# Kernel optimization log

Measured on AMD Instinct MI355X. Metric: run time of the kernel, lower is better.

## Reference

```python
import jax, jax.numpy as jnp
import numpy as np

B, N, C_IN, C_OUT = 8, 4096, 64, 64
NEG_INF = -9e15
LEAKY_SLOPE = 0.01  # torch F.leaky_relu default


def setup_inputs() -> dict:
    key = jax.random.key(0)
    kx, ka, kw, kq, kk = jax.random.split(key, 5)
    X = jax.random.normal(kx, (B, N, C_IN), dtype=jnp.float32)
    A = jax.random.randint(ka, (N, N), 0, 2, dtype=jnp.int32)
    # xavier_uniform with gain=1.414 ~ scaled uniform; plain scaled normal is fine for a numeric reference
    def xavier(k, shape):
        fan_in, fan_out = shape
        bound = 1.414 * np.sqrt(6.0 / (fan_in + fan_out))
        return jax.random.uniform(k, shape, jnp.float32, -bound, bound)
    weight = xavier(kw, (C_IN, C_OUT))
    query = xavier(kq, (C_IN, C_OUT))
    key_p = xavier(kk, (C_IN, C_OUT))
    return {"X": X, "A": A, "weight": weight, "query": query, "key_p": key_p}


def reference(X, A, weight, query, key_p):
    n = X.shape[1]
    idx = jnp.arange(n)
    adj = A.at[idx, idx].set(1)  # add self-loops
    out = jnp.einsum('bni,io->bno', X, weight)
    q = jnp.einsum('bni,io->bno', X, query)
    k = jnp.einsum('bni,io->bno', X, key_p)
    att = jnp.einsum('bnd,bmd->bnm', q, k)          # QK^T, (B,N,N)
    att = jax.nn.leaky_relu(att, LEAKY_SLOPE)
    att = jnp.where(adj[None, :, :] > 0, att, NEG_INF)
    att = jax.nn.softmax(att, axis=-1)
    # dropout p=0 and/or eval mode -> identity
    return jnp.einsum('bnm,bmo->bno', att, out)
```

## Files before the change

kernel.cpp:

```cpp
#include <hip/hip_runtime.h>
#include <stdint.h>

#define BATCH 8
#define NN 4096
#define CC 64
#define MASKV -1.0e30f
#define LOG2E 1.4426950408889634f

typedef _Float16 half8 __attribute__((ext_vector_type(8)));
typedef __fp16 fp16x2 __attribute__((ext_vector_type(2)));
typedef float f32x4 __attribute__((ext_vector_type(4)));
typedef float f32x16 __attribute__((ext_vector_type(16)));

typedef __attribute__((address_space(1))) const unsigned int gu32;
typedef __attribute__((address_space(3))) unsigned int lu32;
#define GLL16(gp, lp) __builtin_amdgcn_global_load_lds( \
    (gu32*)(uintptr_t)(gp), (lu32*)(unsigned)(uintptr_t)(lp), 16, 0, 0)

__device__ __forceinline__ unsigned pk_rtz(float a, float b) {
    union { fp16x2 h; unsigned u; } r;
    r.h = __builtin_amdgcn_cvt_pkrtz(a, b);
    return r.u;
}

__global__ __launch_bounds__(256) void gat_prep(
    const float* __restrict__ X, const float* __restrict__ W0,
    const float* __restrict__ Wq, const float* __restrict__ Wk,
    const int* __restrict__ A,
    _Float16* __restrict__ qh, _Float16* __restrict__ kb,
    _Float16* __restrict__ vt, unsigned short* __restrict__ M16)
{
    __shared__ alignas(16) _Float16 WTh[3][64][72];
    __shared__ alignas(16) _Float16 WTl[3][64][72];
    const int t = threadIdx.x;
    if (blockIdx.x >= 512) {
        const int row = blockIdx.x - 512;
        const int4* ap = (const int4*)(A + (size_t)row * NN + t * 16);
        unsigned m = 0;
        #pragma unroll
        for (int j = 0; j < 4; ++j) {
            int4 a = ap[j];
            m |= (a.x != 0 ? 1u : 0u) << (4*j);
            m |= (a.y != 0 ? 1u : 0u) << (4*j + 1);
            m |= (a.z != 0 ? 1u : 0u) << (4*j + 2);
            m |= (a.w != 0 ? 1u : 0u) << (4*j + 3);
        }
        if (t == (row >> 4)) m |= 1u << (row & 15);
        M16[(size_t)row * 256 + t] = (unsigned short)m;
        return;
    }
    const float* Ws[3] = {W0, Wq, Wk};
    for (int e = t; e < 4096; e += 256) {
        int k = e >> 6, c = e & 63;
        #pragma unroll
        for (int m = 0; m < 3; ++m) {
            float w = Ws[m][e];
            _Float16 hi = (_Float16)w;
            WTh[m][c][k] = hi;
            WTl[m][c][k] = (_Float16)(w - (float)hi);
        }
    }
    __syncthreads();
    const int lane = t & 63, wv = t >> 6;
    const int cl = lane & 15, g = lane >> 4;
    int tile = blockIdx.x * 4 + wv;
    int gr = tile * 16;
    const float* xr = X + (size_t)(gr + cl) * CC;
    half8 xh[2], xl[2];
    #pragma unroll
    for (int kf = 0; kf < 2; ++kf) {
        f32x4 a0 = *(const f32x4*)(xr + g*8 + kf*32);
        f32x4 a1 = *(const f32x4*)(xr + g*8 + kf*32 + 4);
        half8 h, l;
        #pragma unroll
        for (int j = 0; j < 4; ++j) {
            _Float16 h0 = (_Float16)a0[j], h1 = (_Float16)a1[j];
            h[j]   = h0; l[j]   = (_Float16)(a0[j] - (float)h0);
            h[j+4] = h1; l[j+4] = (_Float16)(a1[j] - (float)h1);
        }
        xh[kf] = h; xl[kf] = l;
    }
    #pragma unroll
    for (int mat = 1; mat <= 2; ++mat) {
        #pragma unroll
        for (int nt = 0; nt < 4; ++nt) {
            f32x4 acc = {0.f, 0.f, 0.f, 0.f};
            #pragma unroll
            for (int kf = 0; kf < 2; ++kf) {
                half8 bh = *(const half8*)&WTh[mat][nt*16 + cl][g*8 + kf*32];
                half8 bl = *(const half8*)&WTl[mat][nt*16 + cl][g*8 + kf*32];
                acc = __builtin_amdgcn_mfma_f32_16x16x32_f16(xh[kf], bh, acc, 0, 0, 0);
                acc = __builtin_amdgcn_mfma_f32_16x16x32_f16(xl[kf], bh, acc, 0, 0, 0);
                acc = __builtin_amdgcn_mfma_f32_16x16x32_f16(xh[kf], bl, acc, 0, 0, 0);
            }
            #pragma unroll
            for (int i = 0; i < 4; ++i) {
                size_t off = (size_t)(gr + 4*g + i) * CC + nt*16 + cl;
                if (mat == 1) qh[off] = (_Float16)(acc[i] * LOG2E);
                else          kb[off] = (_Float16)acc[i];
            }
        }
    }
    {
        int b = gr >> 12, n0 = gr & (NN - 1);
        #pragma unroll
        for (int mt = 0; mt < 4; ++mt) {
            f32x4 acc = {0.f, 0.f, 0.f, 0.f};
            #pragma unroll
            for (int kf = 0; kf < 2; ++kf) {
                half8 ah = *(const half8*)&WTh[0][mt*16 + cl][g*8 + kf*32];
                half8 al = *(const half8*)&WTl[0][mt*16 + cl][g*8 + kf*32];
                acc = __builtin_amdgcn_mfma_f32_16x16x32_f16(ah, xh[kf], acc, 0, 0, 0);
                acc = __builtin_amdgcn_mfma_f32_16x16x32_f16(al, xh[kf], acc, 0, 0, 0);
                acc = __builtin_amdgcn_mfma_f32_16x16x32_f16(ah, xl[kf], acc, 0, 0, 0);
            }
            #pragma unroll
            for (int i = 0; i < 4; ++i) {
                int co = mt*16 + 4*g + i;
                vt[((size_t)b * CC + co) * NN + n0 + cl] = (_Float16)acc[i];
            }
        }
    }
}

__global__ __launch_bounds__(256) void gat_attn(
    const _Float16* __restrict__ qg,
    const _Float16* __restrict__ kf16, const _Float16* __restrict__ vtb,
    const unsigned long long* __restrict__ M,
    _Float16* __restrict__ po, float2* __restrict__ pml)
{
    __shared__ alignas(16) _Float16 Kt[2][64][64];
    __shared__ alignas(16) _Float16 Vt[2][64][64];
    __shared__ alignas(8) uint2 LUT[16];
    const int t = threadIdx.x;
    const int lane = t & 63, wv = t >> 6;
    const int q32 = lane & 31, hi = lane >> 5;
    const int blk = blockIdx.x;
    const int b  = blk & 7;
    const int sp = (blk >> 3) & 3;
    const int qb = blk >> 5;
    const int Q0 = qb * 128 + wv * 32;
    const int c0 = sp * 16;
    const int swz = (q32 & 7) << 4;

    if (t < 16) {
        unsigned n = t;
        LUT[n] = make_uint2(((n & 1u) ? 0x0000FFFFu : 0u) | ((n & 2u) ? 0xFFFF0000u : 0u),
                            ((n & 4u) ? 0x0000FFFFu : 0u) | ((n & 8u) ? 0xFFFF0000u : 0u));
    }

    const int lrow = lane >> 3;
    const int lcol = ((lane & 7) * 16) ^ (lrow << 4);
    const bool isK = (wv < 2);
    const int seg = isK ? wv : (wv - 2);
    const char* gsrc0 = isK
        ? (const char*)(kf16 + (size_t)b * NN * CC)
            + (size_t)c0 * 8192 + (size_t)seg * 4096 + lrow * 128 + lcol
        : (const char*)(vtb + (size_t)b * CC * NN)
            + (size_t)c0 * 128 + ((size_t)(seg * 32 + lrow)) * 8192 + lcol;
    const int istride = isK ? 1024 : 65536;
    const int cstride = isK ? 8192 : 128;

    auto stage = [&](int rel, int bufi) {
        const char* s = gsrc0 + (size_t)rel * cstride;
        char* d = isK ? ((char*)&Kt[bufi][0][0] + seg * 4096)
                      : ((char*)&Vt[bufi][0][0] + seg * 4096);
        #pragma unroll
        for (int i = 0; i < 4; ++i)
            GLL16(s + i * istride, d + i * 1024);
    };
    auto pkmax = [](unsigned a, unsigned b) {
        unsigned d;
        asm("v_pk_max_f16 %0, %1, %2" : "=v"(d) : "v"(a), "v"(b));
        return d;
    };

    half8 qf[4];
    {
        const _Float16* qr = qg + ((size_t)b * NN + Q0 + q32) * CC + hi * 8;
        #pragma unroll
        for (int kf = 0; kf < 4; ++kf) qf[kf] = *(const half8*)(qr + kf * 16);
    }
    const unsigned long long* Mrow = M + (size_t)(Q0 + q32) * 64 + c0;

    f32x16 o0 = {}, o1 = {};
    float m_run = 0.f, l_run = 0.f;

    stage(0, 0);
    unsigned long long cm = Mrow[0];
    __syncthreads();

    for (int kc = 0; kc < 16; ++kc) {
        const int cur = kc & 1;
        unsigned long long pmn = 0;
        if (kc < 15) {
            stage(kc + 1, cur ^ 1);
            pmn = Mrow[kc + 1];
        }

        const char* kbase = (const char*)&Kt[cur][0][0] + q32 * 128;
        __builtin_amdgcn_s_setprio(1);
        f32x16 s0 = {}, s1 = {};
        #pragma unroll
        for (int kf = 0; kf < 4; ++kf) {
            const int col = (kf * 32 + hi * 16) ^ swz;
            half8 ka0 = *(const half8*)(kbase + col);
            half8 ka1 = *(const half8*)(kbase + 4096 + col);
            s0 = __builtin_amdgcn_mfma_f32_32x32x16_f16(ka0, qf[kf], s0, 0, 0, 0);
            s1 = __builtin_amdgcn_mfma_f32_32x32x16_f16(ka1, qf[kf], s1, 0, 0, 0);
        }
        __builtin_amdgcn_s_setprio(0);

        const unsigned wlo = (unsigned)cm, whi = (unsigned)(cm >> 32);
        unsigned hm[16];
        #pragma unroll
        for (int kt = 0; kt < 2; ++kt) {
            unsigned w = kt ? whi : wlo;
            #pragma unroll
            for (int a = 0; a < 4; ++a) {
                unsigned nib = (w >> (8 * a + 4 * hi)) & 15u;
                uint2 e = LUT[nib];
                hm[kt*8 + 2*a]     = e.x;
                hm[kt*8 + 2*a + 1] = e.y;
            }
        }
        {
            unsigned sm[16];
            #pragma unroll
            for (int j = 0; j < 8; ++j) {
                sm[j]   = pk_rtz(s0[2*j], s0[2*j+1]) & hm[j];
                sm[8+j] = pk_rtz(s1[2*j], s1[2*j+1]) & hm[8+j];
            }
            unsigned u0 = pkmax(pkmax(pkmax(sm[0],sm[1]),  pkmax(sm[2],sm[3])),
                                pkmax(pkmax(sm[4],sm[5]),  pkmax(sm[6],sm[7])));
            unsigned u1 = pkmax(pkmax(pkmax(sm[8],sm[9]),  pkmax(sm[10],sm[11])),
                                pkmax(pkmax(sm[12],sm[13]),pkmax(sm[14],sm[15])));
            union { unsigned u; fp16x2 h; } tu; tu.u = pkmax(u0, u1);
            float mx = fmaxf(fmaxf((float)tu.h[0], (float)tu.h[1]), 0.f);
            mx = fmaxf(mx, __shfl_xor(mx, 32));
            if (__any(mx > m_run + 8.0f)) {
                float nm = fmaxf(m_run, mx);
                float alpha = __builtin_amdgcn_exp2f(m_run - nm);
                m_run = nm;
                l_run *= alpha;
                #pragma unroll
                for (int i = 0; i < 16; ++i) { o0[i] *= alpha; o1[i] *= alpha; }
            }
        }
        unsigned wp[16];
        #pragma unroll
        for (int j = 0; j < 8; ++j) {
            float p0 = __builtin_amdgcn_exp2f(fmaxf(s0[2*j]   - m_run, fmaf(0.01f, s0[2*j],   -m_run)));
            float p1 = __builtin_amdgcn_exp2f(fmaxf(s0[2*j+1] - m_run, fmaf(0.01f, s0[2*j+1], -m_run)));
            float p2 = __builtin_amdgcn_exp2f(fmaxf(s1[2*j]   - m_run, fmaf(0.01f, s1[2*j],   -m_run)));
            float p3 = __builtin_amdgcn_exp2f(fmaxf(s1[2*j+1] - m_run, fmaf(0.01f, s1[2*j+1], -m_run)));
            wp[j]   = pk_rtz(p0, p1) & hm[j];
            wp[8+j] = pk_rtz(p2, p3) & hm[8+j];
        }
        {
            union { unsigned u; fp16x2 h; } z; z.u = 0u;
            fp16x2 acc = z.h;
            #pragma unroll
            for (int j4 = 0; j4 < 4; ++j4) {
                union { unsigned u; fp16x2 h; } x0, x1, x2, x3;
                x0.u = wp[4*j4]; x1.u = wp[4*j4+1]; x2.u = wp[4*j4+2]; x3.u = wp[4*j4+3];
                acc += (x0.h + x1.h) + (x2.h + x3.h);
            }
            l_run += (float)acc[0] + (float)acc[1];
        }
        #pragma unroll
        for (int g4 = 0; g4 < 4; ++g4) {
            unsigned w0 = wp[4*g4+0], w1 = wp[4*g4+1];
            unsigned w2 = wp[4*g4+2], w3 = wp[4*g4+3];
            unsigned u = hi ? w0 : w2;
            unsigned v = hi ? w1 : w3;
            unsigned su = (unsigned)__shfl_xor((int)u, 32);
            unsigned sv = (unsigned)__shfl_xor((int)v, 32);
            wp[4*g4+0] = hi ? su : w0;
            wp[4*g4+1] = hi ? sv : w1;
            wp[4*g4+2] = hi ? w2 : su;
            wp[4*g4+3] = hi ? w3 : sv;
        }
        const char* vb = (const char*)&Vt[cur][0][0] + q32 * 128;
        __builtin_amdgcn_s_setprio(1);
        #pragma unroll
        for (int kc4 = 0; kc4 < 4; ++kc4) {
            union { unsigned u[4]; half8 h; } pb;
            pb.u[0] = wp[4*kc4+0]; pb.u[1] = wp[4*kc4+1];
            pb.u[2] = wp[4*kc4+2]; pb.u[3] = wp[4*kc4+3];
            const int col = (kc4 * 32 + hi * 16) ^ swz;
            half8 vf0 = *(const half8*)(vb + col);
            half8 vf1 = *(const half8*)(vb + 4096 + col);
            o0 = __builtin_amdgcn_mfma_f32_32x32x16_f16(vf0, pb.h, o0, 0, 0, 0);
            o1 = __builtin_amdgcn_mfma_f32_32x32x16_f16(vf1, pb.h, o1, 0, 0, 0);
        }
        __builtin_amdgcn_s_setprio(0);
        cm = pmn;
        if (kc < 15) __syncthreads();
    }

    float lt = l_run + __shfl_xor(l_run, 32);
    float invl = (lt > 0.f) ? 1.0f / lt : 0.f;
    size_t base = (size_t)sp * (BATCH * NN) + (size_t)b * NN + Q0 + q32;
    _Float16* orow = po + base * 64;
    #pragma unroll
    for (int a = 0; a < 4; ++a) {
        {
            uint2 ow = { pk_rtz(o0[4*a] * invl, o0[4*a+1] * invl),
                         pk_rtz(o0[4*a+2] * invl, o0[4*a+3] * invl) };
            *(uint2*)(orow + 8*a + 4*hi) = ow;
        }
        {
            uint2 ow = { pk_rtz(o1[4*a] * invl, o1[4*a+1] * invl),
                         pk_rtz(o1[4*a+2] * invl, o1[4*a+3] * invl) };
            *(uint2*)(orow + 32 + 8*a + 4*hi) = ow;
        }
    }
    if (hi == 0) pml[base] = make_float2(m_run, lt);
}

__global__ __launch_bounds__(256) void gat_comb(
    const _Float16* __restrict__ po, const float2* __restrict__ pml,
    float* __restrict__ out)
{
    int gid = blockIdx.x * 256 + threadIdx.x;
    int row = gid >> 2;
    int col = (gid & 3) * 16;
    float2 ml[4];
    float Mx = MASKV;
    #pragma unroll
    for (int s = 0; s < 4; ++s) {
        ml[s] = pml[s * (BATCH * NN) + row];
        Mx = fmaxf(Mx, ml[s].x);
    }
    float w[4], den = 0.f;
    #pragma unroll
    for (int s = 0; s < 4; ++s) {
        w[s] = __builtin_amdgcn_exp2f(ml[s].x - Mx) * ml[s].y;
        den += w[s];
    }
    float inv = 1.0f / den;
    float acc[16] = {};
    #pragma unroll
    for (int s = 0; s < 4; ++s) {
        const _Float16* p = po + ((size_t)s * (BATCH * NN) + row) * 64 + col;
        float a = w[s] * inv;
        half8 v0 = *(const half8*)(p);
        half8 v1 = *(const half8*)(p + 8);
        #pragma unroll
        for (int j = 0; j < 8; ++j) {
            acc[j]     += a * (float)v0[j];
            acc[j + 8] += a * (float)v1[j];
        }
    }
    float* op = out + (size_t)row * 64 + col;
    #pragma unroll
    for (int i = 0; i < 4; ++i) {
        f32x4 r = {acc[4*i], acc[4*i+1], acc[4*i+2], acc[4*i+3]};
        *(f32x4*)(op + i*4) = r;
    }
}

extern "C" void kernel_launch(void* const* d_in, const int* in_sizes, int n_in,
                              void* d_out, int out_size, void* d_ws, size_t ws_size,
                              hipStream_t stream) {
    const float* X  = (const float*)d_in[0];
    const int*   A  = (const int*)d_in[1];
    const float* W0 = (const float*)d_in[2];
    const float* Wq = (const float*)d_in[3];
    const float* Wk = (const float*)d_in[4];
    float* out = (float*)d_out;
    char* ws = (char*)d_ws;
    const size_t SZ = (size_t)BATCH * NN * CC * 2;
    _Float16* qh  = (_Float16*)(ws);
    _Float16* kbf = (_Float16*)(ws + SZ);
    _Float16* vtb = (_Float16*)(ws + 2*SZ);
    char* Mbase = ws + 3*SZ;
    _Float16* po = (_Float16*)(Mbase + 2*1024*1024);
    float2* pml  = (float2*)(Mbase + 2*1024*1024 + 4*SZ);

    hipLaunchKernelGGL(gat_prep, dim3(4608), dim3(256), 0, stream,
                       X, W0, Wq, Wk, A, qh, kbf, vtb, (unsigned short*)Mbase);
    hipLaunchKernelGGL(gat_attn, dim3(1024), dim3(256), 0, stream, qh, kbf, vtb,
                       (const unsigned long long*)Mbase, po, pml);
    hipLaunchKernelGGL(gat_comb, dim3(512),  dim3(256), 0, stream, po, pml, out);
}
```

Baseline: 194.4 us.

## Drop LDS staging in attention kernel, load K/V directly from global per wave

The attention kernel becomes one wave per block, with 4096 blocks. It reads K and V fragments straight from global memory into registers instead of staging them through double-buffered LDS with global_load_lds and barriers. This removes the LDS traffic and block-wide synchronisation. In exchange, the four waves that used to share a 128-query block now each fetch the same K/V tiles, which relies on L2/L1 caching, and the K/V loads are no longer prefetched ahead of the MFMAs. The combine kernel is also respread to handle 4 columns per thread with 4x more threads.

```diff
diff --git a/kernel.cpp b/kernel.cpp
--- a/kernel.cpp
+++ b/kernel.cpp
@@ -8,14 +8,10 @@
 #define LOG2E 1.4426950408889634f
 
 typedef _Float16 half8 __attribute__((ext_vector_type(8)));
+typedef _Float16 half4 __attribute__((ext_vector_type(4)));
 typedef __fp16 fp16x2 __attribute__((ext_vector_type(2)));
 typedef float f32x4 __attribute__((ext_vector_type(4)));
 typedef float f32x16 __attribute__((ext_vector_type(16)));
-
-typedef __attribute__((address_space(1))) const unsigned int gu32;
-typedef __attribute__((address_space(3))) unsigned int lu32;
-#define GLL16(gp, lp) __builtin_amdgcn_global_load_lds( \
-    (gu32*)(uintptr_t)(gp), (lu32*)(unsigned)(uintptr_t)(lp), 16, 0, 0)
 
 __device__ __forceinline__ unsigned pk_rtz(float a, float b) {
     union { fp16x2 h; unsigned u; } r;
@@ -123,89 +119,59 @@
     }
 }
 
-__global__ __launch_bounds__(256) void gat_attn(
+__global__ __launch_bounds__(64) void gat_attn(
     const _Float16* __restrict__ qg,
     const _Float16* __restrict__ kf16, const _Float16* __restrict__ vtb,
     const unsigned long long* __restrict__ M,
     _Float16* __restrict__ po, float2* __restrict__ pml)
 {
-    __shared__ alignas(16) _Float16 Kt[2][64][64];
-    __shared__ alignas(16) _Float16 Vt[2][64][64];
     __shared__ alignas(8) uint2 LUT[16];
-    const int t = threadIdx.x;
-    const int lane = t & 63, wv = t >> 6;
+    const int lane = threadIdx.x;
     const int q32 = lane & 31, hi = lane >> 5;
     const int blk = blockIdx.x;
     const int b  = blk & 7;
     const int sp = (blk >> 3) & 3;
-    const int qb = blk >> 5;
-    const int Q0 = qb * 128 + wv * 32;
+    const int Q0 = (blk >> 5) * 32;
     const int c0 = sp * 16;
-    const int swz = (q32 & 7) << 4;
-
-    if (t < 16) {
-        unsigned n = t;
+
+    if (lane < 16) {
+        unsigned n = lane;
         LUT[n] = make_uint2(((n & 1u) ? 0x0000FFFFu : 0u) | ((n & 2u) ? 0xFFFF0000u : 0u),
                             ((n & 4u) ? 0x0000FFFFu : 0u) | ((n & 8u) ? 0xFFFF0000u : 0u));
     }
-
-    const int lrow = lane >> 3;
-    const int lcol = ((lane & 7) * 16) ^ (lrow << 4);
-    const bool isK = (wv < 2);
-    const int seg = isK ? wv : (wv - 2);
-    const char* gsrc0 = isK
-        ? (const char*)(kf16 + (size_t)b * NN * CC)
-            + (size_t)c0 * 8192 + (size_t)seg * 4096 + lrow * 128 + lcol
-        : (const char*)(vtb + (size_t)b * CC * NN)
-            + (size_t)c0 * 128 + ((size_t)(seg * 32 + lrow)) * 8192 + lcol;
-    const int istride = isK ? 1024 : 65536;
-    const int cstride = isK ? 8192 : 128;
-
-    auto stage = [&](int rel, int bufi) {
-        const char* s = gsrc0 + (size_t)rel * cstride;
-        char* d = isK ? ((char*)&Kt[bufi][0][0] + seg * 4096)
-                      : ((char*)&Vt[bufi][0][0] + seg * 4096);
-        #pragma unroll
-        for (int i = 0; i < 4; ++i)
-            GLL16(s + i * istride, d + i * 1024);
-    };
+    __syncthreads();
+
+    half8 qf[4];
+    {
+        const _Float16* qr = qg + ((size_t)b * NN + Q0 + q32) * CC + hi * 8;
+        #pragma unroll
+        for (int kf = 0; kf < 4; ++kf) qf[kf] = *(const half8*)(qr + kf * 16);
+    }
+    const _Float16* kp = kf16 + ((size_t)b * NN + (size_t)c0 * 64 + q32) * CC + hi * 8;
+    const _Float16* vp = vtb + ((size_t)b * CC + q32) * NN + c0 * 64 + hi * 8;
+    const unsigned long long* Mrow = M + (size_t)(Q0 + q32) * 64 + c0;
+
+    f32x16 o0 = {}, o1 = {};
+    float m_run = 0.f, l_run = 0.f;
+
     auto pkmax = [](unsigned a, unsigned b) {
         unsigned d;
         asm("v_pk_max_f16 %0, %1, %2" : "=v"(d) : "v"(a), "v"(b));
         return d;
     };
 
-    half8 qf[4];
-    {
-        const _Float16* qr = qg + ((size_t)b * NN + Q0 + q32) * CC + hi * 8;
-        #pragma unroll
-        for (int kf = 0; kf < 4; ++kf) qf[kf] = *(const half8*)(qr + kf * 16);
-    }
-    const unsigned long long* Mrow = M + (size_t)(Q0 + q32) * 64 + c0;
-
-    f32x16 o0 = {}, o1 = {};
-    float m_run = 0.f, l_run = 0.f;
-
-    stage(0, 0);
     unsigned long long cm = Mrow[0];
-    __syncthreads();
-
     for (int kc = 0; kc < 16; ++kc) {
-        const int cur = kc & 1;
-        unsigned long long pmn = 0;
-        if (kc < 15) {
-            stage(kc + 1, cur ^ 1);
-            pmn = Mrow[kc + 1];
-        }
-
-        const char* kbase = (const char*)&Kt[cur][0][0] + q32 * 128;
+        unsigned long long cmn = 0;
+        if (kc < 15) cmn = Mrow[kc + 1];
+
+        const _Float16* kr = kp + (size_t)kc * 64 * CC;
         __builtin_amdgcn_s_setprio(1);
         f32x16 s0 = {}, s1 = {};
         #pragma unroll
         for (int kf = 0; kf < 4; ++kf) {
-            const int col = (kf * 32 + hi * 16) ^ swz;
-            half8 ka0 = *(const half8*)(kbase + col);
-            half8 ka1 = *(const half8*)(kbase + 4096 + col);
+            half8 ka0 = *(const half8*)(kr + kf * 16);
+            half8 ka1 = *(const half8*)(kr + 32 * CC + kf * 16);
             s0 = __builtin_amdgcn_mfma_f32_32x32x16_f16(ka0, qf[kf], s0, 0, 0, 0);
             s1 = __builtin_amdgcn_mfma_f32_32x32x16_f16(ka1, qf[kf], s1, 0, 0, 0);
         }
@@ -281,22 +247,20 @@
             wp[4*g4+2] = hi ? w2 : su;
             wp[4*g4+3] = hi ? w3 : sv;
         }
-        const char* vb = (const char*)&Vt[cur][0][0] + q32 * 128;
+        const _Float16* vr = vp + kc * 64;
         __builtin_amdgcn_s_setprio(1);
         #pragma unroll
         for (int kc4 = 0; kc4 < 4; ++kc4) {
             union { unsigned u[4]; half8 h; } pb;
             pb.u[0] = wp[4*kc4+0]; pb.u[1] = wp[4*kc4+1];
             pb.u[2] = wp[4*kc4+2]; pb.u[3] = wp[4*kc4+3];
-            const int col = (kc4 * 32 + hi * 16) ^ swz;
-            half8 vf0 = *(const half8*)(vb + col);
-            half8 vf1 = *(const half8*)(vb + 4096 + col);
+            half8 vf0 = *(const half8*)(vr + kc4 * 16);
+            half8 vf1 = *(const half8*)(vr + (size_t)32 * NN + kc4 * 16);
             o0 = __builtin_amdgcn_mfma_f32_32x32x16_f16(vf0, pb.h, o0, 0, 0, 0);
             o1 = __builtin_amdgcn_mfma_f32_32x32x16_f16(vf1, pb.h, o1, 0, 0, 0);
         }
         __builtin_amdgcn_s_setprio(0);
-        cm = pmn;
-        if (kc < 15) __syncthreads();
+        cm = cmn;
     }
 
     float lt = l_run + __shfl_xor(l_run, 32);
@@ -324,8 +288,8 @@
     float* __restrict__ out)
 {
     int gid = blockIdx.x * 256 + threadIdx.x;
-    int row = gid >> 2;
-    int col = (gid & 3) * 16;
+    int row = gid >> 4;
+    int col = (gid & 15) * 4;
     float2 ml[4];
     float Mx = MASKV;
     #pragma unroll
@@ -340,25 +304,17 @@
         den += w[s];
     }
     float inv = 1.0f / den;
-    float acc[16] = {};
+    float acc[4] = {};
     #pragma unroll
     for (int s = 0; s < 4; ++s) {
         const _Float16* p = po + ((size_t)s * (BATCH * NN) + row) * 64 + col;
         float a = w[s] * inv;
-        half8 v0 = *(const half8*)(p);
-        half8 v1 = *(const half8*)(p + 8);
-        #pragma unroll
-        for (int j = 0; j < 8; ++j) {
-            acc[j]     += a * (float)v0[j];
-            acc[j + 8] += a * (float)v1[j];
-        }
-    }
-    float* op = out + (size_t)row * 64 + col;
-    #pragma unroll
-    for (int i = 0; i < 4; ++i) {
-        f32x4 r = {acc[4*i], acc[4*i+1], acc[4*i+2], acc[4*i+3]};
-        *(f32x4*)(op + i*4) = r;
-    }
+        half4 v = *(const half4*)(p);
+        #pragma unroll
+        for (int j = 0; j < 4; ++j) acc[j] += a * (float)v[j];
+    }
+    f32x4 r = {acc[0], acc[1], acc[2], acc[3]};
+    *(f32x4*)(out + (size_t)row * 64 + col) = r;
 }
 
 extern "C" void kernel_launch(void* const* d_in, const int* in_sizes, int n_in,
@@ -381,7 +337,7 @@
 
     hipLaunchKernelGGL(gat_prep, dim3(4608), dim3(256), 0, stream,
                        X, W0, Wq, Wk, A, qh, kbf, vtb, (unsigned short*)Mbase);
-    hipLaunchKernelGGL(gat_attn, dim3(1024), dim3(256), 0, stream, qh, kbf, vtb,
+    hipLaunchKernelGGL(gat_attn, dim3(4096), dim3(64), 0, stream, qh, kbf, vtb,
                        (const unsigned long long*)Mbase, po, pml);
-    hipLaunchKernelGGL(gat_comb, dim3(512),  dim3(256), 0, stream, po, pml, out);
-}
+    hipLaunchKernelGGL(gat_comb, dim3(2048), dim3(256), 0, stream, po, pml, out);
+}
```

New measurement: 248.0 us. +27.6%, slower.

## Triple-buffer K/V tiles and software-pipeline QK^T one chunk ahead; widen combine grid

Applied to the files above, without the earlier changes.

The attention kernel moves from double to triple buffering of the K and V LDS tiles, staging two chunks ahead. It computes the next chunk's QK^T MFMAs before running the softmax and PV of the current chunk, so matrix work can overlap the exp/mask VALU work. This raises LDS use and register pressure because two score accumulators stay live, which may lower occupancy. Separately, the combine kernel is reshaped to four columns per thread with a 4x larger grid, for more parallelism and smaller per-thread loads.

```diff
diff --git a/kernel.cpp b/kernel.cpp
--- a/kernel.cpp
+++ b/kernel.cpp
@@ -8,6 +8,7 @@
 #define LOG2E 1.4426950408889634f
 
 typedef _Float16 half8 __attribute__((ext_vector_type(8)));
+typedef _Float16 half4 __attribute__((ext_vector_type(4)));
 typedef __fp16 fp16x2 __attribute__((ext_vector_type(2)));
 typedef float f32x4 __attribute__((ext_vector_type(4)));
 typedef float f32x16 __attribute__((ext_vector_type(16)));
@@ -129,8 +130,8 @@
     const unsigned long long* __restrict__ M,
     _Float16* __restrict__ po, float2* __restrict__ pml)
 {
-    __shared__ alignas(16) _Float16 Kt[2][64][64];
-    __shared__ alignas(16) _Float16 Vt[2][64][64];
+    __shared__ alignas(16) _Float16 Kt[3][64][64];
+    __shared__ alignas(16) _Float16 Vt[3][64][64];
     __shared__ alignas(8) uint2 LUT[16];
     const int t = threadIdx.x;
     const int lane = t & 63, wv = t >> 6;
@@ -183,24 +184,9 @@
     }
     const unsigned long long* Mrow = M + (size_t)(Q0 + q32) * 64 + c0;
 
-    f32x16 o0 = {}, o1 = {};
-    float m_run = 0.f, l_run = 0.f;
-
-    stage(0, 0);
-    unsigned long long cm = Mrow[0];
-    __syncthreads();
-
-    for (int kc = 0; kc < 16; ++kc) {
-        const int cur = kc & 1;
-        unsigned long long pmn = 0;
-        if (kc < 15) {
-            stage(kc + 1, cur ^ 1);
-            pmn = Mrow[kc + 1];
-        }
-
-        const char* kbase = (const char*)&Kt[cur][0][0] + q32 * 128;
+    auto do_qk = [&](int bufi, f32x16& s0, f32x16& s1) {
+        const char* kbase = (const char*)&Kt[bufi][0][0] + q32 * 128;
         __builtin_amdgcn_s_setprio(1);
-        f32x16 s0 = {}, s1 = {};
         #pragma unroll
         for (int kf = 0; kf < 4; ++kf) {
             const int col = (kf * 32 + hi * 16) ^ swz;
@@ -210,8 +196,25 @@
             s1 = __builtin_amdgcn_mfma_f32_32x32x16_f16(ka1, qf[kf], s1, 0, 0, 0);
         }
         __builtin_amdgcn_s_setprio(0);
-
-        const unsigned wlo = (unsigned)cm, whi = (unsigned)(cm >> 32);
+    };
+
+    f32x16 o0 = {}, o1 = {};
+    float m_run = 0.f, l_run = 0.f;
+
+    stage(0, 0);
+    stage(1, 1);
+    unsigned long long cm0 = Mrow[0], cm1 = Mrow[1], cm2 = 0;
+    __syncthreads();
+
+    f32x16 sc0 = {}, sc1 = {};
+    do_qk(0, sc0, sc1);
+
+    for (int kc = 0; kc < 16; ++kc) {
+        if (kc < 14) { stage(kc + 2, (kc + 2) % 3); cm2 = Mrow[kc + 2]; }
+        f32x16 sn0 = {}, sn1 = {};
+        if (kc < 15) do_qk((kc + 1) % 3, sn0, sn1);
+
+        const unsigned wlo = (unsigned)cm0, whi = (unsigned)(cm0 >> 32);
         unsigned hm[16];
         #pragma unroll
         for (int kt = 0; kt < 2; ++kt) {
@@ -228,8 +231,8 @@
             unsigned sm[16];
             #pragma unroll
             for (int j = 0; j < 8; ++j) {
-                sm[j]   = pk_rtz(s0[2*j], s0[2*j+1]) & hm[j];
-                sm[8+j] = pk_rtz(s1[2*j], s1[2*j+1]) & hm[8+j];
+                sm[j]   = pk_rtz(sc0[2*j], sc0[2*j+1]) & hm[j];
+                sm[8+j] = pk_rtz(sc1[2*j], sc1[2*j+1]) & hm[8+j];
             }
             unsigned u0 = pkmax(pkmax(pkmax(sm[0],sm[1]),  pkmax(sm[2],sm[3])),
                                 pkmax(pkmax(sm[4],sm[5]),  pkmax(sm[6],sm[7])));
@@ -250,10 +253,10 @@
         unsigned wp[16];
         #pragma unroll
         for (int j = 0; j < 8; ++j) {
-            float p0 = __builtin_amdgcn_exp2f(fmaxf(s0[2*j]   - m_run, fmaf(0.01f, s0[2*j],   -m_run)));
-            float p1 = __builtin_amdgcn_exp2f(fmaxf(s0[2*j+1] - m_run, fmaf(0.01f, s0[2*j+1], -m_run)));
-            float p2 = __builtin_amdgcn_exp2f(fmaxf(s1[2*j]   - m_run, fmaf(0.01f, s1[2*j],   -m_run)));
-            float p3 = __builtin_amdgcn_exp2f(fmaxf(s1[2*j+1] - m_run, fmaf(0.01f, s1[2*j+1], -m_run)));
+            float p0 = __builtin_amdgcn_exp2f(fmaxf(sc0[2*j]   - m_run, fmaf(0.01f, sc0[2*j],   -m_run)));
+            float p1 = __builtin_amdgcn_exp2f(fmaxf(sc0[2*j+1] - m_run, fmaf(0.01f, sc0[2*j+1], -m_run)));
+            float p2 = __builtin_amdgcn_exp2f(fmaxf(sc1[2*j]   - m_run, fmaf(0.01f, sc1[2*j],   -m_run)));
+            float p3 = __builtin_amdgcn_exp2f(fmaxf(sc1[2*j+1] - m_run, fmaf(0.01f, sc1[2*j+1], -m_run)));
             wp[j]   = pk_rtz(p0, p1) & hm[j];
             wp[8+j] = pk_rtz(p2, p3) & hm[8+j];
         }
@@ -281,7 +284,7 @@
             wp[4*g4+2] = hi ? w2 : su;
             wp[4*g4+3] = hi ? w3 : sv;
         }
-        const char* vb = (const char*)&Vt[cur][0][0] + q32 * 128;
+        const char* vb = (const char*)&Vt[kc % 3][0][0] + q32 * 128;
         __builtin_amdgcn_s_setprio(1);
         #pragma unroll
         for (int kc4 = 0; kc4 < 4; ++kc4) {
@@ -295,7 +298,8 @@
             o1 = __builtin_amdgcn_mfma_f32_32x32x16_f16(vf1, pb.h, o1, 0, 0, 0);
         }
         __builtin_amdgcn_s_setprio(0);
-        cm = pmn;
+        cm0 = cm1; cm1 = cm2;
+        sc0 = sn0; sc1 = sn1;
         if (kc < 15) __syncthreads();
     }
 
@@ -324,8 +328,8 @@
     float* __restrict__ out)
 {
     int gid = blockIdx.x * 256 + threadIdx.x;
-    int row = gid >> 2;
-    int col = (gid & 3) * 16;
+    int row = gid >> 4;
+    int col = (gid & 15) * 4;
     float2 ml[4];
     float Mx = MASKV;
     #pragma unroll
@@ -340,25 +344,17 @@
         den += w[s];
     }
     float inv = 1.0f / den;
-    float acc[16] = {};
+    float acc[4] = {};
     #pragma unroll
     for (int s = 0; s < 4; ++s) {
         const _Float16* p = po + ((size_t)s * (BATCH * NN) + row) * 64 + col;
         float a = w[s] * inv;
-        half8 v0 = *(const half8*)(p);
-        half8 v1 = *(const half8*)(p + 8);
-        #pragma unroll
-        for (int j = 0; j < 8; ++j) {
-            acc[j]     += a * (float)v0[j];
-            acc[j + 8] += a * (float)v1[j];
-        }
-    }
-    float* op = out + (size_t)row * 64 + col;
-    #pragma unroll
-    for (int i = 0; i < 4; ++i) {
-        f32x4 r = {acc[4*i], acc[4*i+1], acc[4*i+2], acc[4*i+3]};
-        *(f32x4*)(op + i*4) = r;
-    }
+        half4 v = *(const half4*)(p);
+        #pragma unroll
+        for (int j = 0; j < 4; ++j) acc[j] += a * (float)v[j];
+    }
+    f32x4 r = {acc[0], acc[1], acc[2], acc[3]};
+    *(f32x4*)(out + (size_t)row * 64 + col) = r;
 }
 
 extern "C" void kernel_launch(void* const* d_in, const int* in_sizes, int n_in,
@@ -383,5 +379,5 @@
                        X, W0, Wq, Wk, A, qh, kbf, vtb, (unsigned short*)Mbase);
     hipLaunchKernelGGL(gat_attn, dim3(1024), dim3(256), 0, stream, qh, kbf, vtb,
                        (const unsigned long long*)Mbase, po, pml);
-    hipLaunchKernelGGL(gat_comb, dim3(512),  dim3(256), 0, stream, po, pml, out);
-}
+    hipLaunchKernelGGL(gat_comb, dim3(2048), dim3(256), 0, stream, po, pml, out);
+}
```

Measured after the change: 194.4 us. About the same (-0.0%).
